# Performance work log

Measured on AMD Instinct MI355X. Metric: run time of the kernel, lower is better.

The kernel has to match this reference:

```python
import jax, jax.numpy as jnp
import numpy as np

B, NUM_USERS, NUM_ITEMS = 128, 10000, 8192
HID, LAT, NEMB, NQ, NRES = 256, 64, 512, 4, 2
CC = 0.25


def conv1d(x, w, b, stride, pad):
    # x: [N, C_in, L], w: [C_out, C_in, K] (torch Conv1d layout)
    out = jax.lax.conv_general_dilated(
        x, w, window_strides=(stride,), padding=[(pad, pad)],
        dimension_numbers=('NCH', 'OIH', 'NCH'))
    return out + b[None, :, None]


def convT1d(x, w, b, stride, pad):
    # w: [C_in, C_out, K] (torch ConvTranspose1d layout); equivalent conv with
    # flipped kernel, lhs dilation = stride, padding = K-1-pad.
    k = w.shape[-1]
    w_conv = jnp.flip(w, -1).transpose(1, 0, 2)  # [C_out, C_in, K]
    p = k - 1 - pad
    out = jax.lax.conv_general_dilated(
        x, w_conv, window_strides=(1,), padding=[(p, p)],
        lhs_dilation=(stride,), dimension_numbers=('NCH', 'OIH', 'NCH'))
    return out + b[None, :, None]


def res_block(x, w1, b1, w2, b2):
    out = jax.nn.relu(conv1d(x, w1, b1, 1, 1))
    out = conv1d(out, w2, b2, 1, 0)
    return jax.nn.relu(out + x)


def vq_step(inputs, codebook):
    # inputs: [B, LAT, L]; faithful to torch: view(-1, embedding_dim) row-major
    flat = inputs.reshape(-1, codebook.shape[1])  # [M, 64]
    dist = (jnp.sum(flat ** 2, axis=1, keepdims=True)
            + jnp.sum(codebook ** 2, axis=1)
            - 2.0 * flat @ codebook.T)  # [M, NEMB]
    idx = jnp.argmin(dist, axis=1)  # [M]
    quant = codebook[idx].reshape(inputs.shape)  # gather == onehot @ codebook
    e_loss = jnp.mean((jax.lax.stop_gradient(quant) - inputs) ** 2)
    q_loss = jnp.mean((quant - jax.lax.stop_gradient(inputs)) ** 2)
    loss = q_loss + CC * e_loss
    quant_st = inputs + jax.lax.stop_gradient(quant - inputs)  # straight-through
    counts = jnp.zeros((codebook.shape[0],), jnp.float32).at[idx].add(1.0)
    avg = counts / flat.shape[0]
    perp = jnp.exp(-jnp.sum(avg * jnp.log(avg + 1e-10)))
    return quant_st, loss, perp


def setup_inputs() -> dict:
    key = jax.random.key(0)
    ks = iter(jax.random.split(key, 32))
    nk = lambda: next(ks)
    w = lambda shape: (jax.random.normal(nk(), shape, jnp.float32) * 0.05)
    inp = {
        'user_ids': jax.random.randint(nk(), (B,), 0, NUM_USERS),
        'interaction_matrix': jax.random.uniform(nk(), (NUM_USERS, NUM_ITEMS), jnp.float32),
        'enc_conv_w': w((HID, 1, 4)), 'enc_conv_b': jnp.zeros((HID,), jnp.float32),
        'enc_res_w1': w((NRES, HID, HID, 3)), 'enc_res_b1': jnp.zeros((NRES, HID), jnp.float32),
        'enc_res_w2': w((NRES, HID, HID, 1)), 'enc_res_b2': jnp.zeros((NRES, HID), jnp.float32),
        'enc_final_w': w((LAT, HID, 3)), 'enc_final_b': jnp.zeros((LAT,), jnp.float32),
        'codebooks': jax.random.uniform(nk(), (NQ, NEMB, LAT), jnp.float32,
                                        minval=-1.0 / NEMB, maxval=1.0 / NEMB),
        'dec_convT_w': w((LAT, HID, 4)), 'dec_convT_b': jnp.zeros((HID,), jnp.float32),
        'dec_res_w1': w((NRES, HID, HID, 3)), 'dec_res_b1': jnp.zeros((NRES, HID), jnp.float32),
        'dec_res_w2': w((NRES, HID, HID, 1)), 'dec_res_b2': jnp.zeros((NRES, HID), jnp.float32),
        'dec_finalT_w': w((HID, 1, 3)), 'dec_finalT_b': jnp.zeros((1,), jnp.float32),
        'out_proj_w': (jax.random.normal(nk(), (NUM_ITEMS, NUM_ITEMS), jnp.float32)
                       * (1.0 / np.sqrt(NUM_ITEMS))),
        'out_proj_b': jnp.zeros((NUM_ITEMS,), jnp.float32),
    }
    return inp


def reference(user_ids, interaction_matrix, enc_conv_w, enc_conv_b,
              enc_res_w1, enc_res_b1, enc_res_w2, enc_res_b2,
              enc_final_w, enc_final_b, codebooks,
              dec_convT_w, dec_convT_b, dec_res_w1, dec_res_b1,
              dec_res_w2, dec_res_b2, dec_finalT_w, dec_finalT_b,
              out_proj_w, out_proj_b):
    x = interaction_matrix[user_ids][:, None, :]  # [B, 1, NUM_ITEMS]; dropout in eval mode = identity
    h = jax.nn.relu(conv1d(x, enc_conv_w, enc_conv_b, 2, 1))  # [B, HID, L]
    for i in range(NRES):
        h = res_block(h, enc_res_w1[i], enc_res_b1[i], enc_res_w2[i], enc_res_b2[i])
    z_e = conv1d(h, enc_final_w, enc_final_b, 1, 1)  # [B, LAT, L]

    residual = z_e
    z_q = jnp.zeros_like(z_e)
    vq_loss = jnp.float32(0.0)
    perps = []
    for q in range(NQ):
        quant, loss, perp = vq_step(residual, codebooks[q])
        residual = residual - quant
        z_q = z_q + quant
        vq_loss = vq_loss + loss
        perps.append(perp)
    perplexity = jnp.mean(jnp.stack(perps))

    d = jax.nn.relu(convT1d(z_q, dec_convT_w, dec_convT_b, 2, 1))  # [B, HID, NUM_ITEMS]
    for i in range(NRES):
        d = res_block(d, dec_res_w1[i], dec_res_b1[i], dec_res_w2[i], dec_res_b2[i])
    d = convT1d(d, dec_finalT_w, dec_finalT_b, 1, 1)[:, 0, :]  # [B, NUM_ITEMS]
    recon = d @ out_proj_w.T + out_proj_b
    return recon, vq_loss, perplexity
```

## Files before the change

kernel.cpp:

```cpp
#include <hip/hip_runtime.h>
#include <math.h>

#define NB 128
#define NITEMS 8192
#define NHID 256
#define NLAT 64
#define NEMB_ 512
#define NQ_ 4
#define LENC 4096
#define LDEC 8192
#define NROWS 524288
#define VQ_NELEM 33554432.0f
#define KC_ 4

typedef unsigned short u16;
typedef __attribute__((ext_vector_type(8))) short bf16x8;
typedef __attribute__((ext_vector_type(4))) float f32x4;

__device__ __forceinline__ u16 f2b(float f){
  unsigned u = __float_as_uint(f);
  unsigned r = (u + 0x7FFFu + ((u>>16)&1u)) >> 16;
  return (u16)r;
}
__device__ __forceinline__ float b2f(u16 h){
  return __uint_as_float(((unsigned)h)<<16);
}

__global__ void k_zero(float* __restrict__ p, int n){
  int i = blockIdx.x*256 + threadIdx.x;
  if(i < n) p[i] = 0.f;
}

__global__ void k_gather(const int* __restrict__ uid, const float* __restrict__ mat,
                         float* __restrict__ x){
  int b = blockIdx.y;
  int i = blockIdx.x*256 + threadIdx.x;
  x[(size_t)b*NITEMS + i] = mat[(size_t)uid[b]*NITEMS + i];
}

__global__ void k_packw(const float* __restrict__ w, u16* __restrict__ wb,
                        int CO, int CI, int K){
  int idx = blockIdx.x*256 + threadIdx.x;
  int n = CO*CI*K;
  if(idx >= n) return;
  int k  = idx % K;
  int ci = (idx / K) % CI;
  int co = idx / (K*CI);
  wb[((size_t)k*CO + co)*CI + ci] = f2b(w[idx]);
}

__global__ void k_packwT(const float* __restrict__ w, u16* __restrict__ wb){
  int idx = blockIdx.x*256 + threadIdx.x;
  if(idx >= 64*256*4) return;
  int k  = idx % 4;
  int co = (idx / 4) % 256;
  int ci = idx / (4*256);
  wb[((size_t)k*256 + co)*64 + ci] = f2b(w[idx]);
}

__global__ void k_cbsplit(const float* __restrict__ cb, u16* __restrict__ h,
                          u16* __restrict__ l){
  int idx = blockIdx.x*256 + threadIdx.x;
  float v = -2.0f*cb[idx];
  u16 hh = f2b(v);
  h[idx] = hh;
  l[idx] = f2b(v - b2f(hh));
}

__global__ void k_cbnorm(const float* __restrict__ cb, float* __restrict__ cb2){
  int idx = blockIdx.x*256 + threadIdx.x;
  if(idx >= NQ_*NEMB_) return;
  const float* p = cb + (size_t)idx*64;
  float s = 0.f;
  #pragma unroll
  for(int d=0; d<64; d++) s = fmaf(p[d], p[d], s);
  cb2[idx] = s;
}

__global__ void k_packdv(const float* __restrict__ d, u16* __restrict__ h,
                         u16* __restrict__ l){
  int i = blockIdx.x*256 + threadIdx.x;
  float v = d[i];
  u16 hh = f2b(v);
  h[i] = hh;
  l[i] = f2b(v - b2f(hh));
}

__global__ __launch_bounds__(256) void k_enc0(
    const float* __restrict__ x, const float* __restrict__ w,
    const float* __restrict__ bias, u16* __restrict__ out){
  const int co = threadIdx.x;
  const int b  = blockIdx.y;
  const int l0 = blockIdx.x*16;
  const float* xr = x + (size_t)b*NITEMS;
  float4 wv = *(const float4*)&w[co*4];
  float bv = bias[co];
  for(int dl=0; dl<16; dl++){
    int l = l0 + dl;
    int i0 = 2*l - 1;
    float x0 = (i0 >= 0) ? xr[i0] : 0.f;
    float x1 = xr[i0+1];
    float x2 = xr[i0+2];
    float x3 = (i0+3 < NITEMS) ? xr[i0+3] : 0.f;
    float acc = bv;
    acc = fmaf(wv.x, x0, acc); acc = fmaf(wv.y, x1, acc);
    acc = fmaf(wv.z, x2, acc); acc = fmaf(wv.w, x3, acc);
    out[((size_t)(b*LENC + l))*NHID + co] = f2b(fmaxf(acc, 0.f));
  }
}

#define LP 40
template<int CIN, int COUT, int KK, int WM, int WN, int RELU, int RES, int CHF>
__global__ __launch_bounds__(256) void k_cgemm(
    const u16* __restrict__ in, const u16* __restrict__ wb,
    const float* __restrict__ bias, const u16* __restrict__ res,
    void* __restrict__ outv, int L){
  constexpr int CO_T = WM*64;
  constexpr int LT   = WN*64;
  constexpr int PAD  = (KK-1)/2;
  constexpr int RXS  = LT + KK - 1;
  __shared__ __align__(16) u16 sx[RXS][LP];
  __shared__ __align__(16) u16 sw[KK][CO_T][LP];

  const int tid = threadIdx.x;
  const int bb  = blockIdx.z;
  const int co0 = blockIdx.y*CO_T;
  const int l0  = blockIdx.x*LT;
  const int wave = tid>>6, lane = tid&63;
  const int wm = wave % WM, wn = wave / WM;
  const int quad = lane>>4, l16 = lane&15;

  f32x4 acc[4][4];
  #pragma unroll
  for(int m=0;m<4;m++)
    #pragma unroll
    for(int n=0;n<4;n++) acc[m][n] = (f32x4){0.f,0.f,0.f,0.f};

  for(int cib=0; cib<CIN; cib+=32){
    for(int s=tid; s<RXS*4; s+=256){
      int row = s>>2, ch = s&3;
      int l = l0 - PAD + row;
      int4 v;
      if(l >= 0 && l < L)
        v = *(const int4*)(in + ((size_t)(bb*L + l))*CIN + cib + ch*8);
      else
        v = make_int4(0,0,0,0);
      *(int4*)&sx[row][ch*8] = v;
    }
    for(int s=tid; s<KK*CO_T*4; s+=256){
      int row = s>>2, ch = s&3;
      int kk = row / CO_T, cr = row % CO_T;
      int4 v = *(const int4*)(wb + ((size_t)(kk*COUT + co0 + cr))*CIN + cib + ch*8);
      *(int4*)&sw[kk][cr][ch*8] = v;
    }
    __syncthreads();
    #pragma unroll
    for(int kk=0; kk<KK; kk++){
      bf16x8 af[4];
      #pragma unroll
      for(int m=0;m<4;m++)
        af[m] = *(const bf16x8*)&sw[kk][wm*64 + m*16 + l16][quad*8];
      #pragma unroll
      for(int n=0;n<4;n++){
        bf16x8 bf = *(const bf16x8*)&sx[wn*64 + n*16 + l16 + kk][quad*8];
        #pragma unroll
        for(int m=0;m<4;m++)
          acc[m][n] = __builtin_amdgcn_mfma_f32_16x16x32_bf16(af[m], bf, acc[m][n], 0,0,0);
      }
    }
    __syncthreads();
  }

  #pragma unroll
  for(int m=0;m<4;m++){
    int co4 = co0 + wm*64 + m*16 + quad*4;
    float4 bv = *(const float4*)&bias[co4];
    #pragma unroll
    for(int n=0;n<4;n++){
      int l = l0 + wn*64 + n*16 + l16;
      float v0 = acc[m][n][0] + bv.x;
      float v1 = acc[m][n][1] + bv.y;
      float v2 = acc[m][n][2] + bv.z;
      float v3 = acc[m][n][3] + bv.w;
      if(RES){
        ushort4 rv = *(const ushort4*)(res + ((size_t)(bb*L + l))*COUT + co4);
        v0 += b2f(rv.x); v1 += b2f(rv.y); v2 += b2f(rv.z); v3 += b2f(rv.w);
      }
      if(RELU){
        v0 = fmaxf(v0,0.f); v1 = fmaxf(v1,0.f); v2 = fmaxf(v2,0.f); v3 = fmaxf(v3,0.f);
      }
      if(CHF){
        float* of = (float*)outv;
        of[((size_t)(bb*COUT + co4+0))*L + l] = v0;
        of[((size_t)(bb*COUT + co4+1))*L + l] = v1;
        of[((size_t)(bb*COUT + co4+2))*L + l] = v2;
        of[((size_t)(bb*COUT + co4+3))*L + l] = v3;
      }else{
        u16* ob = (u16*)outv;
        ushort4 o;
        o.x = f2b(v0); o.y = f2b(v1); o.z = f2b(v2); o.w = f2b(v3);
        *(ushort4*)(ob + ((size_t)(bb*L + l))*COUT + co4) = o;
      }
    }
  }
}

__global__ __launch_bounds__(256) void k_vq(
    const float* __restrict__ z_e, const float* __restrict__ cb,
    const u16* __restrict__ cbh, const u16* __restrict__ cbl,
    const float* __restrict__ cb2,
    float* __restrict__ z_q, float* __restrict__ loss, int* __restrict__ counts){
  __shared__ int hist[NQ_][NEMB_];
  __shared__ float sloss[NQ_];
  const int tid = threadIdx.x;
  for(int i=tid;i<NQ_*NEMB_;i+=256) (&hist[0][0])[i]=0;
  if(tid < NQ_) sloss[tid] = 0.f;
  __syncthreads();

  const int lane = tid & 63, wave = tid >> 6;
  const int quad = lane >> 4, l16 = lane & 15;
  const size_t row0 = (size_t)blockIdx.x*128 + (size_t)wave*32;

  bf16x8 vbh[2][2], vbl[2][2];
  float qa[2][2][8];
  #pragma unroll
  for(int bt=0;bt<2;bt++){
    #pragma unroll
    for(int ks=0;ks<2;ks++){
      const float* zp = z_e + (row0 + bt*16 + l16)*64 + ks*32 + quad*8;
      float4 v0 = *(const float4*)zp;
      float4 v1 = *(const float4*)(zp+4);
      float f[8] = {v0.x,v0.y,v0.z,v0.w,v1.x,v1.y,v1.z,v1.w};
      #pragma unroll
      for(int j=0;j<8;j++){
        u16 h = f2b(f[j]);
        vbh[bt][ks][j] = (short)h;
        vbl[bt][ks][j] = (short)f2b(f[j] - b2f(h));
        qa[bt][ks][j] = 0.f;
      }
    }
  }

  #pragma unroll 1
  for(int q=0;q<NQ_;q++){
    const u16* Ah = cbh + (size_t)q*NEMB_*64 + (size_t)l16*64 + quad*8;
    const u16* Al = cbl + (size_t)q*NEMB_*64 + (size_t)l16*64 + quad*8;
    const float* c2q = cb2 + q*NEMB_;

    float rq0 = 0.f, rq1 = 0.f;
    #pragma unroll
    for(int ks=0;ks<2;ks++)
      #pragma unroll
      for(int j=0;j<8;j++){
        float r0 = b2f((u16)vbh[0][ks][j]) + b2f((u16)vbl[0][ks][j]);
        float r1 = b2f((u16)vbh[1][ks][j]) + b2f((u16)vbl[1][ks][j]);
        rq0 = fmaf(r0,r0,rq0); rq1 = fmaf(r1,r1,rq1);
      }

    float best0 = 3.0e38f, best1 = 3.0e38f;
    int bi0 = 0, bi1 = 0;

    bf16x8 cah0 = *(const bf16x8*)(Ah);
    bf16x8 cah1 = *(const bf16x8*)(Ah + 32);
    bf16x8 cal0 = *(const bf16x8*)(Al);
    bf16x8 cal1 = *(const bf16x8*)(Al + 32);
    #pragma unroll 1
    for(int t=0;t<32;t++){
      int tn = (t < 31) ? (t+1) : 31;
      const u16* nh = Ah + (size_t)tn*1024;
      const u16* nl = Al + (size_t)tn*1024;
      bf16x8 nah0 = *(const bf16x8*)(nh);
      bf16x8 nah1 = *(const bf16x8*)(nh + 32);
      bf16x8 nal0 = *(const bf16x8*)(nl);
      bf16x8 nal1 = *(const bf16x8*)(nl + 32);

      f32x4 acc0 = (f32x4){0.f,0.f,0.f,0.f};
      f32x4 acc1 = (f32x4){0.f,0.f,0.f,0.f};
      acc0 = __builtin_amdgcn_mfma_f32_16x16x32_bf16(cah0, vbh[0][0], acc0, 0,0,0);
      acc1 = __builtin_amdgcn_mfma_f32_16x16x32_bf16(cah0, vbh[1][0], acc1, 0,0,0);
      acc0 = __builtin_amdgcn_mfma_f32_16x16x32_bf16(cah0, vbl[0][0], acc0, 0,0,0);
      acc1 = __builtin_amdgcn_mfma_f32_16x16x32_bf16(cah0, vbl[1][0], acc1, 0,0,0);
      acc0 = __builtin_amdgcn_mfma_f32_16x16x32_bf16(cal0, vbh[0][0], acc0, 0,0,0);
      acc1 = __builtin_amdgcn_mfma_f32_16x16x32_bf16(cal0, vbh[1][0], acc1, 0,0,0);
      acc0 = __builtin_amdgcn_mfma_f32_16x16x32_bf16(cah1, vbh[0][1], acc0, 0,0,0);
      acc1 = __builtin_amdgcn_mfma_f32_16x16x32_bf16(cah1, vbh[1][1], acc1, 0,0,0);
      acc0 = __builtin_amdgcn_mfma_f32_16x16x32_bf16(cah1, vbl[0][1], acc0, 0,0,0);
      acc1 = __builtin_amdgcn_mfma_f32_16x16x32_bf16(cah1, vbl[1][1], acc1, 0,0,0);
      acc0 = __builtin_amdgcn_mfma_f32_16x16x32_bf16(cal1, vbh[0][1], acc0, 0,0,0);
      acc1 = __builtin_amdgcn_mfma_f32_16x16x32_bf16(cal1, vbh[1][1], acc1, 0,0,0);

      float4 c2v = *(const float4*)(c2q + t*16 + quad*4);
      float c2a[4] = {c2v.x, c2v.y, c2v.z, c2v.w};
      #pragma unroll
      for(int i=0;i<4;i++){
        int code = t*16 + quad*4 + i;
        float d0 = acc0[i] + c2a[i];
        float d1 = acc1[i] + c2a[i];
        if(d0 < best0){ best0 = d0; bi0 = code; }
        if(d1 < best1){ best1 = d1; bi1 = code; }
      }
      cah0 = nah0; cah1 = nah1; cal0 = nal0; cal1 = nal1;
    }

    #pragma unroll
    for(int off=16; off<=32; off<<=1){
      float ob0 = __shfl_xor(best0, off); int oi0 = __shfl_xor(bi0, off);
      float ob1 = __shfl_xor(best1, off); int oi1 = __shfl_xor(bi1, off);
      if(ob0 < best0 || (ob0 == best0 && oi0 < bi0)){ best0 = ob0; bi0 = oi0; }
      if(ob1 < best1 || (ob1 == best1 && oi1 < bi1)){ best1 = ob1; bi1 = oi1; }
      rq0 += __shfl_xor(rq0, off);
      rq1 += __shfl_xor(rq1, off);
    }

    float v = (rq0 + best0) + (rq1 + best1);
    #pragma unroll
    for(int off=1; off<=8; off<<=1) v += __shfl_xor(v, off);
    if(lane == 0) atomicAdd(&sloss[q], v);
    if(quad == 0){
      atomicAdd(&hist[q][bi0], 1);
      atomicAdd(&hist[q][bi1], 1);
    }

    #pragma unroll
    for(int bt=0;bt<2;bt++){
      int bi = bt ? bi1 : bi0;
      const float* cp = cb + ((size_t)q*NEMB_ + bi)*64 + quad*8;
      #pragma unroll
      for(int ks=0;ks<2;ks++){
        float4 c0 = *(const float4*)(cp + ks*32);
        float4 c1 = *(const float4*)(cp + ks*32 + 4);
        float cf[8] = {c0.x,c0.y,c0.z,c0.w,c1.x,c1.y,c1.z,c1.w};
        #pragma unroll
        for(int j=0;j<8;j++){
          float r = b2f((u16)vbh[bt][ks][j]) + b2f((u16)vbl[bt][ks][j]) - cf[j];
          u16 h = f2b(r);
          vbh[bt][ks][j] = (short)h;
          vbl[bt][ks][j] = (short)f2b(r - b2f(h));
          qa[bt][ks][j] += cf[j];
        }
      }
    }
  }

  #pragma unroll
  for(int bt=0;bt<2;bt++)
    #pragma unroll
    for(int ks=0;ks<2;ks++){
      float* zp = z_q + (row0 + bt*16 + l16)*64 + ks*32 + quad*8;
      float4 w0 = {qa[bt][ks][0], qa[bt][ks][1], qa[bt][ks][2], qa[bt][ks][3]};
      float4 w1 = {qa[bt][ks][4], qa[bt][ks][5], qa[bt][ks][6], qa[bt][ks][7]};
      *(float4*)zp = w0;
      *(float4*)(zp+4) = w1;
    }

  __syncthreads();
  if(tid < NQ_) atomicAdd(&loss[tid], sloss[tid]);
  for(int i=tid;i<NQ_*NEMB_;i+=256){
    int v = (&hist[0][0])[i];
    if(v) atomicAdd(&counts[i], v);
  }
}

__global__ __launch_bounds__(256) void k_convT(
    const float* __restrict__ zq, const u16* __restrict__ wb4,
    const float* __restrict__ bias, u16* __restrict__ out){
  __shared__ __align__(16) u16 sxT[66][LP];
  __shared__ __align__(16) u16 sw4[4][128][LP];
  const int tid = threadIdx.x;
  const int bb  = blockIdx.z;
  const int co0 = blockIdx.y*128;
  const int t0  = blockIdx.x*64;
  const int wave = tid>>6, lane = tid&63;
  const int wm = wave & 1, wn = wave >> 1;
  const int quad = lane>>4, l16 = lane&15;

  f32x4 ae[4][2], ao[4][2];
  #pragma unroll
  for(int m=0;m<4;m++)
    #pragma unroll
    for(int n=0;n<2;n++){ ae[m][n]=(f32x4){0,0,0,0}; ao[m][n]=(f32x4){0,0,0,0}; }

  for(int cib=0; cib<NLAT; cib+=32){
    for(int s=tid; s<66*32; s+=256){
      int ci = s/66, tt = s%66;
      int t = t0 - 1 + tt;
      float v = 0.f;
      if(t >= 0 && t < LENC) v = zq[((size_t)(bb*NLAT + cib + ci))*LENC + t];
      sxT[tt][ci] = f2b(v);
    }
    for(int s=tid; s<4*128*4; s+=256){
      int row = s>>2, ch = s&3;
      int tap = row>>7, cr = row&127;
      int4 v = *(const int4*)(wb4 + ((size_t)(tap*NHID + co0 + cr))*NLAT + cib + ch*8);
      *(int4*)&sw4[tap][cr][ch*8] = v;
    }
    __syncthreads();
    #pragma unroll
    for(int m=0;m<4;m++){
      int crow = wm*64 + m*16 + l16;
      bf16x8 a0 = *(const bf16x8*)&sw4[0][crow][quad*8];
      bf16x8 a1 = *(const bf16x8*)&sw4[1][crow][quad*8];
      bf16x8 a2 = *(const bf16x8*)&sw4[2][crow][quad*8];
      bf16x8 a3 = *(const bf16x8*)&sw4[3][crow][quad*8];
      #pragma unroll
      for(int n=0;n<2;n++){
        int off = wn*32 + n*16 + l16;
        bf16x8 bm = *(const bf16x8*)&sxT[off  ][quad*8];
        bf16x8 b0 = *(const bf16x8*)&sxT[off+1][quad*8];
        bf16x8 bp = *(const bf16x8*)&sxT[off+2][quad*8];
        ae[m][n] = __builtin_amdgcn_mfma_f32_16x16x32_bf16(a1, b0, ae[m][n], 0,0,0);
        ae[m][n] = __builtin_amdgcn_mfma_f32_16x16x32_bf16(a3, bm, ae[m][n], 0,0,0);
        ao[m][n] = __builtin_amdgcn_mfma_f32_16x16x32_bf16(a2, b0, ao[m][n], 0,0,0);
        ao[m][n] = __builtin_amdgcn_mfma_f32_16x16x32_bf16(a0, bp, ao[m][n], 0,0,0);
      }
    }
    __syncthreads();
  }

  #pragma unroll
  for(int m=0;m<4;m++){
    int co4 = co0 + wm*64 + m*16 + quad*4;
    float4 bv = *(const float4*)&bias[co4];
    #pragma unroll
    for(int n=0;n<2;n++){
      int t = t0 + wn*32 + n*16 + l16;
      int je = 2*t, jo = 2*t+1;
      ushort4 oe, oo;
      oe.x = f2b(fmaxf(ae[m][n][0]+bv.x, 0.f));
      oe.y = f2b(fmaxf(ae[m][n][1]+bv.y, 0.f));
      oe.z = f2b(fmaxf(ae[m][n][2]+bv.z, 0.f));
      oe.w = f2b(fmaxf(ae[m][n][3]+bv.w, 0.f));
      oo.x = f2b(fmaxf(ao[m][n][0]+bv.x, 0.f));
      oo.y = f2b(fmaxf(ao[m][n][1]+bv.y, 0.f));
      oo.z = f2b(fmaxf(ao[m][n][2]+bv.z, 0.f));
      oo.w = f2b(fmaxf(ao[m][n][3]+bv.w, 0.f));
      *(ushort4*)(out + ((size_t)(bb*LDEC + je))*NHID + co4) = oe;
      *(ushort4*)(out + ((size_t)(bb*LDEC + jo))*NHID + co4) = oo;
    }
  }
}

__global__ __launch_bounds__(256) void k_finalT(
    const u16* __restrict__ in, const float* __restrict__ w,
    const float* __restrict__ bias, float* __restrict__ out){
  __shared__ u16 sd[66][258];
  __shared__ float red[4][64];
  const int tid = threadIdx.x;
  const int j0 = blockIdx.x*64;
  const int bb = blockIdx.y;
  for(int s=tid; s<66*32; s+=256){
    int row = s>>5, ch = s&31;
    int l = j0 - 1 + row;
    int4 v = make_int4(0,0,0,0);
    if(l >= 0 && l < LDEC)
      v = *(const int4*)(in + ((size_t)(bb*LDEC + l))*NHID + ch*8);
    int* dst = (int*)&sd[row][ch*8];
    dst[0]=v.x; dst[1]=v.y; dst[2]=v.z; dst[3]=v.w;
  }
  __syncthreads();
  const int jl = tid & 63;
  const int part = tid >> 6;
  float acc = 0.f;
  for(int ci=0; ci<64; ci++){
    int cg = part*64 + ci;
    float w0 = w[cg*3+2], w1 = w[cg*3+1], w2 = w[cg*3+0];
    acc = fmaf(w0, b2f(sd[jl  ][cg]), acc);
    acc = fmaf(w1, b2f(sd[jl+1][cg]), acc);
    acc = fmaf(w2, b2f(sd[jl+2][cg]), acc);
  }
  red[part][jl] = acc;
  __syncthreads();
  if(tid < 64)
    out[(size_t)bb*NITEMS + j0 + tid] =
      bias[0] + red[0][tid] + red[1][tid] + red[2][tid] + red[3][tid];
}

__global__ __launch_bounds__(256) void k_opmm(
    const u16* __restrict__ dvh, const u16* __restrict__ dvl,
    const float* __restrict__ Wm, float* __restrict__ part){
  const int tid = threadIdx.x;
  const int wave = tid>>6, lane = tid&63;
  const int quad = lane>>4, l16 = lane&15;
  const int wb_ = wave & 1;
  const int wn_ = wave >> 1;
  const int n0 = blockIdx.x*64;
  const int kz = blockIdx.y;
  const int n_wave = n0 + wn_*32;

  f32x4 acc[4][2];
  #pragma unroll
  for(int bt=0;bt<4;bt++)
    #pragma unroll
    for(int nt=0;nt<2;nt++) acc[bt][nt] = (f32x4){0.f,0.f,0.f,0.f};

  const size_t abase = (size_t)(wb_*64 + l16)*NITEMS + quad*8;
  const size_t wrow  = (size_t)(n_wave + l16)*NITEMS + quad*8;
  const int kbase = kz*(NITEMS/KC_);

  #pragma unroll 2
  for(int t=0; t<(NITEMS/KC_)/32; t++){
    const int k = kbase + t*32;
    bf16x8 ah[4], al[4];
    #pragma unroll
    for(int bt=0;bt<4;bt++){
      ah[bt] = *(const bf16x8*)(dvh + abase + (size_t)bt*16*NITEMS + k);
      al[bt] = *(const bf16x8*)(dvl + abase + (size_t)bt*16*NITEMS + k);
    }
    #pragma unroll
    for(int nt=0;nt<2;nt++){
      const float* wp = Wm + wrow + (size_t)nt*16*NITEMS + k;
      float4 wa = *(const float4*)wp;
      float4 wc = *(const float4*)(wp+4);
      float f[8] = {wa.x,wa.y,wa.z,wa.w,wc.x,wc.y,wc.z,wc.w};
      bf16x8 wh, wl;
      #pragma unroll
      for(int j=0;j<8;j++){
        u16 h = f2b(f[j]);
        wh[j] = (short)h;
        wl[j] = (short)f2b(f[j] - b2f(h));
      }
      #pragma unroll
      for(int bt=0;bt<4;bt++){
        acc[bt][nt] = __builtin_amdgcn_mfma_f32_16x16x32_bf16(ah[bt], wh, acc[bt][nt], 0,0,0);
        acc[bt][nt] = __builtin_amdgcn_mfma_f32_16x16x32_bf16(al[bt], wh, acc[bt][nt], 0,0,0);
        acc[bt][nt] = __builtin_amdgcn_mfma_f32_16x16x32_bf16(ah[bt], wl, acc[bt][nt], 0,0,0);
        acc[bt][nt] = __builtin_amdgcn_mfma_f32_16x16x32_bf16(al[bt], wl, acc[bt][nt], 0,0,0);
      }
    }
  }

  float* pp = part + (size_t)kz*NB*NITEMS;
  #pragma unroll
  for(int bt=0;bt<4;bt++){
    const int brow = wb_*64 + bt*16 + quad*4;
    #pragma unroll
    for(int nt=0;nt<2;nt++){
      const int n = n_wave + nt*16 + l16;
      #pragma unroll
      for(int i=0;i<4;i++)
        pp[(size_t)(brow+i)*NITEMS + n] = acc[bt][nt][i];
    }
  }
}

__global__ __launch_bounds__(256) void k_opred(
    const float* __restrict__ part, const float* __restrict__ bias,
    float* __restrict__ out){
  const size_t i = ((size_t)blockIdx.x*256 + threadIdx.x)*4;
  float4 s = *(const float4*)&bias[(int)(i & (NITEMS-1))];
  #pragma unroll
  for(int kz=0;kz<KC_;kz++){
    float4 p = *(const float4*)&part[(size_t)kz*NB*NITEMS + i];
    s.x+=p.x; s.y+=p.y; s.z+=p.z; s.w+=p.w;
  }
  *(float4*)&out[i] = s;
}

__global__ void k_finalize(const float* __restrict__ loss, const int* __restrict__ counts,
                           float* __restrict__ out){
  __shared__ float sh[512];
  const int tid = threadIdx.x;
  float perp_sum = 0.f;
  for(int q=0;q<NQ_;q++){
    float avg = (float)counts[q*NEMB_+tid] / (float)NROWS;
    sh[tid] = avg*logf(avg + 1e-10f);
    __syncthreads();
    for(int s=256;s>0;s>>=1){ if(tid<s) sh[tid]+=sh[tid+s]; __syncthreads(); }
    if(tid==0) perp_sum += expf(-sh[0]);
    __syncthreads();
  }
  if(tid==0){
    float vl = 0.f;
    for(int q=0;q<NQ_;q++) vl += 1.25f*loss[q]/VQ_NELEM;
    out[0] = vl;
    out[1] = perp_sum/(float)NQ_;
  }
}

extern "C" void kernel_launch(void* const* d_in, const int* in_sizes, int n_in,
                              void* d_out, int out_size, void* d_ws, size_t ws_size,
                              hipStream_t stream){
  (void)in_sizes; (void)n_in; (void)out_size;
  const int*   uid   = (const int*)d_in[0];
  const float* mat   = (const float*)d_in[1];
  const float* ec_w  = (const float*)d_in[2];
  const float* ec_b  = (const float*)d_in[3];
  const float* er_w1 = (const float*)d_in[4];
  const float* er_b1 = (const float*)d_in[5];
  const float* er_w2 = (const float*)d_in[6];
  const float* er_b2 = (const float*)d_in[7];
  const float* ef_w  = (const float*)d_in[8];
  const float* ef_b  = (const float*)d_in[9];
  const float* cb    = (const float*)d_in[10];
  const float* dt_w  = (const float*)d_in[11];
  const float* dt_b  = (const float*)d_in[12];
  const float* dr_w1 = (const float*)d_in[13];
  const float* dr_b1 = (const float*)d_in[14];
  const float* dr_w2 = (const float*)d_in[15];
  const float* dr_b2 = (const float*)d_in[16];
  const float* df_w  = (const float*)d_in[17];
  const float* df_b  = (const float*)d_in[18];
  const float* op_w  = (const float*)d_in[19];
  const float* op_b  = (const float*)d_in[20];
  float* outp = (float*)d_out;

  float* W = (float*)d_ws;
  size_t o = 0;
  float* xg    = W + o; o += (size_t)NB*NITEMS;
  float* dvec  = W + o; o += (size_t)NB*NITEMS;
  u16* wb3e0 = (u16*)(W + o); o += 3*NHID*NHID/2;
  u16* wb3e1 = (u16*)(W + o); o += 3*NHID*NHID/2;
  u16* wb3d0 = (u16*)(W + o); o += 3*NHID*NHID/2;
  u16* wb3d1 = (u16*)(W + o); o += 3*NHID*NHID/2;
  u16* wbF   = (u16*)(W + o); o += 3*NLAT*NHID/2;
  u16* wb1e0 = (u16*)(W + o); o += NHID*NHID/2;
  u16* wb1e1 = (u16*)(W + o); o += NHID*NHID/2;
  u16* wb1d0 = (u16*)(W + o); o += NHID*NHID/2;
  u16* wb1d1 = (u16*)(W + o); o += NHID*NHID/2;
  u16* wbT   = (u16*)(W + o); o += 4*NLAT*NHID/2;
  u16* cbh   = (u16*)(W + o); o += (size_t)NQ_*NEMB_*64/2;
  u16* cbl   = (u16*)(W + o); o += (size_t)NQ_*NEMB_*64/2;
  float* cb2   = W + o; o += NQ_*NEMB_;
  float* lossb = W + o; o += 4;
  int*   counts= (int*)(W + o); o += NQ_*NEMB_;
  u16* dvh   = (u16*)(W + o); o += (size_t)NB*NITEMS/2;
  u16* dvl   = (u16*)(W + o); o += (size_t)NB*NITEMS/2;
  float* partb = W + o; o += (size_t)KC_*NB*NITEMS;
  const size_t fixedF = o;

  const size_t perBF = (size_t)LDEC*NHID/2;
  size_t availF = ws_size/sizeof(float) > fixedF ? ws_size/sizeof(float) - fixedF : 0;
  int CB = 128;
  while(CB > 1 && (size_t)CB*2*perBF > availF) CB >>= 1;

  k_zero<<<(4 + NQ_*NEMB_ + 255)/256,256,0,stream>>>(lossb, 4 + NQ_*NEMB_);

  k_packw<<<(3*NHID*NHID+255)/256,256,0,stream>>>(er_w1,             wb3e0, NHID, NHID, 3);
  k_packw<<<(3*NHID*NHID+255)/256,256,0,stream>>>(er_w1+3*NHID*NHID, wb3e1, NHID, NHID, 3);
  k_packw<<<(3*NHID*NHID+255)/256,256,0,stream>>>(dr_w1,             wb3d0, NHID, NHID, 3);
  k_packw<<<(3*NHID*NHID+255)/256,256,0,stream>>>(dr_w1+3*NHID*NHID, wb3d1, NHID, NHID, 3);
  k_packw<<<(3*NLAT*NHID+255)/256,256,0,stream>>>(ef_w,              wbF,   NLAT, NHID, 3);
  k_packw<<<(NHID*NHID+255)/256,256,0,stream>>>(er_w2,               wb1e0, NHID, NHID, 1);
  k_packw<<<(NHID*NHID+255)/256,256,0,stream>>>(er_w2+NHID*NHID,     wb1e1, NHID, NHID, 1);
  k_packw<<<(NHID*NHID+255)/256,256,0,stream>>>(dr_w2,               wb1d0, NHID, NHID, 1);
  k_packw<<<(NHID*NHID+255)/256,256,0,stream>>>(dr_w2+NHID*NHID,     wb1d1, NHID, NHID, 1);
  k_packwT<<<(4*NLAT*NHID+255)/256,256,0,stream>>>(dt_w, wbT);
  k_cbsplit<<<(NQ_*NEMB_*64)/256,256,0,stream>>>(cb, cbh, cbl);
  k_cbnorm<<<(NQ_*NEMB_+255)/256,256,0,stream>>>(cb, cb2);

  k_gather<<<dim3(NITEMS/256, NB),256,0,stream>>>(uid, mat, xg);

  u16* D0b = (u16*)(W + fixedF);
  u16* D1b = D0b + (size_t)CB*LDEC*NHID;

  for(int c0 = 0; c0 < NB; c0 += CB){
    u16* E0 = D0b;
    u16* E1 = D0b + (size_t)CB*LENC*NHID;
    float* z_e = (float*)D1b;
    float* z_q = z_e + (size_t)CB*NLAT*LENC;
    const float* xgc = xg + (size_t)c0*NITEMS;
    float* dvc = dvec + (size_t)c0*NITEMS;

    k_enc0<<<dim3(LENC/16, CB),256,0,stream>>>(xgc, ec_w, ec_b, E0);
    k_cgemm<256,256,3,2,2,1,0,0><<<dim3(LENC/128, 2, CB),256,0,stream>>>(E0, wb3e0, er_b1,      nullptr, E1, LENC);
    k_cgemm<256,256,1,2,2,1,1,0><<<dim3(LENC/128, 2, CB),256,0,stream>>>(E1, wb1e0, er_b2,      E0,      E0, LENC);
    k_cgemm<256,256,3,2,2,1,0,0><<<dim3(LENC/128, 2, CB),256,0,stream>>>(E0, wb3e1, er_b1+NHID, nullptr, E1, LENC);
    k_cgemm<256,256,1,2,2,1,1,0><<<dim3(LENC/128, 2, CB),256,0,stream>>>(E1, wb1e1, er_b2+NHID, E0,      E0, LENC);
    k_cgemm<256, 64,3,1,4,0,0,1><<<dim3(LENC/256, 1, CB),256,0,stream>>>(E0, wbF,   ef_b,       nullptr, z_e, LENC);

    k_vq<<<CB*32,256,0,stream>>>(z_e, cb, cbh, cbl, cb2, z_q, lossb, counts);

    k_convT<<<dim3(LENC/64, 2, CB),256,0,stream>>>(z_q, wbT, dt_b, D0b);
    k_cgemm<256,256,3,2,2,1,0,0><<<dim3(LDEC/128, 2, CB),256,0,stream>>>(D0b, wb3d0, dr_b1,      nullptr, D1b, LDEC);
    k_cgemm<256,256,1,2,2,1,1,0><<<dim3(LDEC/128, 2, CB),256,0,stream>>>(D1b, wb1d0, dr_b2,      D0b,     D0b, LDEC);
    k_cgemm<256,256,3,2,2,1,0,0><<<dim3(LDEC/128, 2, CB),256,0,stream>>>(D0b, wb3d1, dr_b1+NHID, nullptr, D1b, LDEC);
    k_cgemm<256,256,1,2,2,1,1,0><<<dim3(LDEC/128, 2, CB),256,0,stream>>>(D1b, wb1d1, dr_b2+NHID, D0b,     D0b, LDEC);
    k_finalT<<<dim3(LDEC/64, CB),256,0,stream>>>(D0b, df_w, df_b, dvc);
  }

  k_packdv<<<NB*NITEMS/256,256,0,stream>>>(dvec, dvh, dvl);
  k_opmm<<<dim3(NITEMS/64, KC_),256,0,stream>>>(dvh, dvl, op_w, partb);
  k_opred<<<NB*NITEMS/1024,256,0,stream>>>(partb, op_b, outp);
  k_finalize<<<1,512,0,stream>>>(lossb, counts, outp + (size_t)NB*NITEMS);
}
```

Baseline: 6.859 ms.

## Process 64 rows per wave in VQ with triple-buffered codebook loads

The VQ kernel now handles four 16-row tiles per wave instead of two, so each codebook fragment load feeds twice as many MFMAs, and the grid is halved to match. Codebook tiles are prefetched through a three-stage rotating register buffer instead of single-step double buffering. The per-row quantized accumulator is dropped; z_q is rebuilt at the end as z_e minus the final residual, which trades registers for an extra reload of z_e. Register pressure rises and occupancy may fall, and the reconstructed z_q may differ slightly in rounding from the old running sum.

New measurement: 6.477 ms. 1.06x faster.

```diff
diff --git a/kernel.cpp b/kernel.cpp
--- a/kernel.cpp
+++ b/kernel.cpp
@@ -205,6 +205,57 @@
   }
 }
 
+#define VQ_LOADT(S, T) { \
+  const u16* nh_ = Ah + (size_t)(T)*1024; \
+  const u16* nl_ = Al + (size_t)(T)*1024; \
+  s_h0[S] = *(const bf16x8*)(nh_); \
+  s_h1[S] = *(const bf16x8*)(nh_ + 32); \
+  s_l0[S] = *(const bf16x8*)(nl_); \
+  s_l1[S] = *(const bf16x8*)(nl_ + 32); \
+}
+
+#define VQ_DOT(S, T) { \
+  f32x4 ac0=(f32x4){0.f,0.f,0.f,0.f}, ac1=ac0, ac2=ac0, ac3=ac0; \
+  ac0 = __builtin_amdgcn_mfma_f32_16x16x32_bf16(s_h0[S], vbh[0][0], ac0,0,0,0); \
+  ac1 = __builtin_amdgcn_mfma_f32_16x16x32_bf16(s_h0[S], vbh[1][0], ac1,0,0,0); \
+  ac2 = __builtin_amdgcn_mfma_f32_16x16x32_bf16(s_h0[S], vbh[2][0], ac2,0,0,0); \
+  ac3 = __builtin_amdgcn_mfma_f32_16x16x32_bf16(s_h0[S], vbh[3][0], ac3,0,0,0); \
+  ac0 = __builtin_amdgcn_mfma_f32_16x16x32_bf16(s_h0[S], vbl[0][0], ac0,0,0,0); \
+  ac1 = __builtin_amdgcn_mfma_f32_16x16x32_bf16(s_h0[S], vbl[1][0], ac1,0,0,0); \
+  ac2 = __builtin_amdgcn_mfma_f32_16x16x32_bf16(s_h0[S], vbl[2][0], ac2,0,0,0); \
+  ac3 = __builtin_amdgcn_mfma_f32_16x16x32_bf16(s_h0[S], vbl[3][0], ac3,0,0,0); \
+  ac0 = __builtin_amdgcn_mfma_f32_16x16x32_bf16(s_l0[S], vbh[0][0], ac0,0,0,0); \
+  ac1 = __builtin_amdgcn_mfma_f32_16x16x32_bf16(s_l0[S], vbh[1][0], ac1,0,0,0); \
+  ac2 = __builtin_amdgcn_mfma_f32_16x16x32_bf16(s_l0[S], vbh[2][0], ac2,0,0,0); \
+  ac3 = __builtin_amdgcn_mfma_f32_16x16x32_bf16(s_l0[S], vbh[3][0], ac3,0,0,0); \
+  ac0 = __builtin_amdgcn_mfma_f32_16x16x32_bf16(s_h1[S], vbh[0][1], ac0,0,0,0); \
+  ac1 = __builtin_amdgcn_mfma_f32_16x16x32_bf16(s_h1[S], vbh[1][1], ac1,0,0,0); \
+  ac2 = __builtin_amdgcn_mfma_f32_16x16x32_bf16(s_h1[S], vbh[2][1], ac2,0,0,0); \
+  ac3 = __builtin_amdgcn_mfma_f32_16x16x32_bf16(s_h1[S], vbh[3][1], ac3,0,0,0); \
+  ac0 = __builtin_amdgcn_mfma_f32_16x16x32_bf16(s_h1[S], vbl[0][1], ac0,0,0,0); \
+  ac1 = __builtin_amdgcn_mfma_f32_16x16x32_bf16(s_h1[S], vbl[1][1], ac1,0,0,0); \
+  ac2 = __builtin_amdgcn_mfma_f32_16x16x32_bf16(s_h1[S], vbl[2][1], ac2,0,0,0); \
+  ac3 = __builtin_amdgcn_mfma_f32_16x16x32_bf16(s_h1[S], vbl[3][1], ac3,0,0,0); \
+  ac0 = __builtin_amdgcn_mfma_f32_16x16x32_bf16(s_l1[S], vbh[0][1], ac0,0,0,0); \
+  ac1 = __builtin_amdgcn_mfma_f32_16x16x32_bf16(s_l1[S], vbh[1][1], ac1,0,0,0); \
+  ac2 = __builtin_amdgcn_mfma_f32_16x16x32_bf16(s_l1[S], vbh[2][1], ac2,0,0,0); \
+  ac3 = __builtin_amdgcn_mfma_f32_16x16x32_bf16(s_l1[S], vbh[3][1], ac3,0,0,0); \
+  float4 c2v = *(const float4*)(c2q + (T)*16 + quad*4); \
+  const float* c2a = (const float*)&c2v; \
+  _Pragma("unroll") \
+  for(int i_=0;i_<4;i_++){ \
+    int code = (T)*16 + quad*4 + i_; \
+    float d0 = ac0[i_] + c2a[i_]; \
+    float d1 = ac1[i_] + c2a[i_]; \
+    float d2 = ac2[i_] + c2a[i_]; \
+    float d3 = ac3[i_] + c2a[i_]; \
+    if(d0 < best[0]){ best[0]=d0; bi[0]=code; } \
+    if(d1 < best[1]){ best[1]=d1; bi[1]=code; } \
+    if(d2 < best[2]){ best[2]=d2; bi[2]=code; } \
+    if(d3 < best[3]){ best[3]=d3; bi[3]=code; } \
+  } \
+}
+
 __global__ __launch_bounds__(256) void k_vq(
     const float* __restrict__ z_e, const float* __restrict__ cb,
     const u16* __restrict__ cbh, const u16* __restrict__ cbl,
@@ -219,12 +270,11 @@
 
   const int lane = tid & 63, wave = tid >> 6;
   const int quad = lane >> 4, l16 = lane & 15;
-  const size_t row0 = (size_t)blockIdx.x*128 + (size_t)wave*32;
-
-  bf16x8 vbh[2][2], vbl[2][2];
-  float qa[2][2][8];
-  #pragma unroll
-  for(int bt=0;bt<2;bt++){
+  const size_t row0 = (size_t)blockIdx.x*256 + (size_t)wave*64;
+
+  bf16x8 vbh[4][2], vbl[4][2];
+  #pragma unroll
+  for(int bt=0;bt<4;bt++){
     #pragma unroll
     for(int ks=0;ks<2;ks++){
       const float* zp = z_e + (row0 + bt*16 + l16)*64 + ks*32 + quad*8;
@@ -236,7 +286,6 @@
         u16 h = f2b(f[j]);
         vbh[bt][ks][j] = (short)h;
         vbl[bt][ks][j] = (short)f2b(f[j] - b2f(h));
-        qa[bt][ks][j] = 0.f;
       }
     }
   }
@@ -247,84 +296,59 @@
     const u16* Al = cbl + (size_t)q*NEMB_*64 + (size_t)l16*64 + quad*8;
     const float* c2q = cb2 + q*NEMB_;
 
-    float rq0 = 0.f, rq1 = 0.f;
-    #pragma unroll
-    for(int ks=0;ks<2;ks++)
-      #pragma unroll
-      for(int j=0;j<8;j++){
-        float r0 = b2f((u16)vbh[0][ks][j]) + b2f((u16)vbl[0][ks][j]);
-        float r1 = b2f((u16)vbh[1][ks][j]) + b2f((u16)vbl[1][ks][j]);
-        rq0 = fmaf(r0,r0,rq0); rq1 = fmaf(r1,r1,rq1);
-      }
-
-    float best0 = 3.0e38f, best1 = 3.0e38f;
-    int bi0 = 0, bi1 = 0;
-
-    bf16x8 cah0 = *(const bf16x8*)(Ah);
-    bf16x8 cah1 = *(const bf16x8*)(Ah + 32);
-    bf16x8 cal0 = *(const bf16x8*)(Al);
-    bf16x8 cal1 = *(const bf16x8*)(Al + 32);
+    float rq[4];
+    #pragma unroll
+    for(int bt=0;bt<4;bt++){
+      float s = 0.f;
+      #pragma unroll
+      for(int ks=0;ks<2;ks++)
+        #pragma unroll
+        for(int j=0;j<8;j++){
+          float r = b2f((u16)vbh[bt][ks][j]) + b2f((u16)vbl[bt][ks][j]);
+          s = fmaf(r,r,s);
+        }
+      rq[bt] = s;
+    }
+
+    float best[4] = {3.0e38f,3.0e38f,3.0e38f,3.0e38f};
+    int   bi[4]   = {0,0,0,0};
+
+    bf16x8 s_h0[3], s_h1[3], s_l0[3], s_l1[3];
+    VQ_LOADT(0, 0);
+    VQ_LOADT(1, 1);
     #pragma unroll 1
-    for(int t=0;t<32;t++){
-      int tn = (t < 31) ? (t+1) : 31;
-      const u16* nh = Ah + (size_t)tn*1024;
-      const u16* nl = Al + (size_t)tn*1024;
-      bf16x8 nah0 = *(const bf16x8*)(nh);
-      bf16x8 nah1 = *(const bf16x8*)(nh + 32);
-      bf16x8 nal0 = *(const bf16x8*)(nl);
-      bf16x8 nal1 = *(const bf16x8*)(nl + 32);
-
-      f32x4 acc0 = (f32x4){0.f,0.f,0.f,0.f};
-      f32x4 acc1 = (f32x4){0.f,0.f,0.f,0.f};
-      acc0 = __builtin_amdgcn_mfma_f32_16x16x32_bf16(cah0, vbh[0][0], acc0, 0,0,0);
-      acc1 = __builtin_amdgcn_mfma_f32_16x16x32_bf16(cah0, vbh[1][0], acc1, 0,0,0);
-      acc0 = __builtin_amdgcn_mfma_f32_16x16x32_bf16(cah0, vbl[0][0], acc0, 0,0,0);
-      acc1 = __builtin_amdgcn_mfma_f32_16x16x32_bf16(cah0, vbl[1][0], acc1, 0,0,0);
-      acc0 = __builtin_amdgcn_mfma_f32_16x16x32_bf16(cal0, vbh[0][0], acc0, 0,0,0);
-      acc1 = __builtin_amdgcn_mfma_f32_16x16x32_bf16(cal0, vbh[1][0], acc1, 0,0,0);
-      acc0 = __builtin_amdgcn_mfma_f32_16x16x32_bf16(cah1, vbh[0][1], acc0, 0,0,0);
-      acc1 = __builtin_amdgcn_mfma_f32_16x16x32_bf16(cah1, vbh[1][1], acc1, 0,0,0);
-      acc0 = __builtin_amdgcn_mfma_f32_16x16x32_bf16(cah1, vbl[0][1], acc0, 0,0,0);
-      acc1 = __builtin_amdgcn_mfma_f32_16x16x32_bf16(cah1, vbl[1][1], acc1, 0,0,0);
-      acc0 = __builtin_amdgcn_mfma_f32_16x16x32_bf16(cal1, vbh[0][1], acc0, 0,0,0);
-      acc1 = __builtin_amdgcn_mfma_f32_16x16x32_bf16(cal1, vbh[1][1], acc1, 0,0,0);
-
-      float4 c2v = *(const float4*)(c2q + t*16 + quad*4);
-      float c2a[4] = {c2v.x, c2v.y, c2v.z, c2v.w};
-      #pragma unroll
-      for(int i=0;i<4;i++){
-        int code = t*16 + quad*4 + i;
-        float d0 = acc0[i] + c2a[i];
-        float d1 = acc1[i] + c2a[i];
-        if(d0 < best0){ best0 = d0; bi0 = code; }
-        if(d1 < best1){ best1 = d1; bi1 = code; }
-      }
-      cah0 = nah0; cah1 = nah1; cal0 = nal0; cal1 = nal1;
-    }
-
-    #pragma unroll
-    for(int off=16; off<=32; off<<=1){
-      float ob0 = __shfl_xor(best0, off); int oi0 = __shfl_xor(bi0, off);
-      float ob1 = __shfl_xor(best1, off); int oi1 = __shfl_xor(bi1, off);
-      if(ob0 < best0 || (ob0 == best0 && oi0 < bi0)){ best0 = ob0; bi0 = oi0; }
-      if(ob1 < best1 || (ob1 == best1 && oi1 < bi1)){ best1 = ob1; bi1 = oi1; }
-      rq0 += __shfl_xor(rq0, off);
-      rq1 += __shfl_xor(rq1, off);
-    }
-
-    float v = (rq0 + best0) + (rq1 + best1);
+    for(int t=0; t<30; t+=3){
+      VQ_LOADT(2, t+2);  VQ_DOT(0, t);
+      VQ_LOADT(0, t+3);  VQ_DOT(1, t+1);
+      VQ_LOADT(1, t+4);  VQ_DOT(2, t+2);
+    }
+    VQ_DOT(0, 30);
+    VQ_DOT(1, 31);
+
+    #pragma unroll
+    for(int bt=0;bt<4;bt++){
+      #pragma unroll
+      for(int off=16; off<=32; off<<=1){
+        float ob = __shfl_xor(best[bt], off); int oi = __shfl_xor(bi[bt], off);
+        if(ob < best[bt] || (ob == best[bt] && oi < bi[bt])){ best[bt]=ob; bi[bt]=oi; }
+        rq[bt] += __shfl_xor(rq[bt], off);
+      }
+    }
+
+    float v = (rq[0]+best[0]) + (rq[1]+best[1]) + (rq[2]+best[2]) + (rq[3]+best[3]);
     #pragma unroll
     for(int off=1; off<=8; off<<=1) v += __shfl_xor(v, off);
     if(lane == 0) atomicAdd(&sloss[q], v);
     if(quad == 0){
-      atomicAdd(&hist[q][bi0], 1);
-      atomicAdd(&hist[q][bi1], 1);
-    }
-
-    #pragma unroll
-    for(int bt=0;bt<2;bt++){
-      int bi = bt ? bi1 : bi0;
-      const float* cp = cb + ((size_t)q*NEMB_ + bi)*64 + quad*8;
+      atomicAdd(&hist[q][bi[0]], 1);
+      atomicAdd(&hist[q][bi[1]], 1);
+      atomicAdd(&hist[q][bi[2]], 1);
+      atomicAdd(&hist[q][bi[3]], 1);
+    }
+
+    #pragma unroll
+    for(int bt=0;bt<4;bt++){
+      const float* cp = cb + ((size_t)q*NEMB_ + bi[bt])*64 + quad*8;
       #pragma unroll
       for(int ks=0;ks<2;ks++){
         float4 c0 = *(const float4*)(cp + ks*32);
@@ -336,22 +360,30 @@
           u16 h = f2b(r);
           vbh[bt][ks][j] = (short)h;
           vbl[bt][ks][j] = (short)f2b(r - b2f(h));
-          qa[bt][ks][j] += cf[j];
         }
       }
     }
   }
 
   #pragma unroll
-  for(int bt=0;bt<2;bt++)
+  for(int bt=0;bt<4;bt++){
     #pragma unroll
     for(int ks=0;ks<2;ks++){
-      float* zp = z_q + (row0 + bt*16 + l16)*64 + ks*32 + quad*8;
-      float4 w0 = {qa[bt][ks][0], qa[bt][ks][1], qa[bt][ks][2], qa[bt][ks][3]};
-      float4 w1 = {qa[bt][ks][4], qa[bt][ks][5], qa[bt][ks][6], qa[bt][ks][7]};
-      *(float4*)zp = w0;
-      *(float4*)(zp+4) = w1;
-    }
+      const float* zp = z_e + (row0 + bt*16 + l16)*64 + ks*32 + quad*8;
+      float*       qp = z_q + (row0 + bt*16 + l16)*64 + ks*32 + quad*8;
+      float4 z0 = *(const float4*)zp;
+      float4 z1 = *(const float4*)(zp+4);
+      float zf[8] = {z0.x,z0.y,z0.z,z0.w,z1.x,z1.y,z1.z,z1.w};
+      float o[8];
+      #pragma unroll
+      for(int j=0;j<8;j++)
+        o[j] = zf[j] - (b2f((u16)vbh[bt][ks][j]) + b2f((u16)vbl[bt][ks][j]));
+      float4 w0 = {o[0],o[1],o[2],o[3]};
+      float4 w1 = {o[4],o[5],o[6],o[7]};
+      *(float4*)qp = w0;
+      *(float4*)(qp+4) = w1;
+    }
+  }
 
   __syncthreads();
   if(tid < NQ_) atomicAdd(&loss[tid], sloss[tid]);
@@ -668,7 +700,7 @@
     k_cgemm<256,256,1,2,2,1,1,0><<<dim3(LENC/128, 2, CB),256,0,stream>>>(E1, wb1e1, er_b2+NHID, E0,      E0, LENC);
     k_cgemm<256, 64,3,1,4,0,0,1><<<dim3(LENC/256, 1, CB),256,0,stream>>>(E0, wbF,   ef_b,       nullptr, z_e, LENC);
 
-    k_vq<<<CB*32,256,0,stream>>>(z_e, cb, cbh, cbl, cb2, z_q, lossb, counts);
+    k_vq<<<CB*16,256,0,stream>>>(z_e, cb, cbh, cbl, cb2, z_q, lossb, counts);
 
     k_convT<<<dim3(LENC/64, 2, CB),256,0,stream>>>(z_q, wbT, dt_b, D0b);
     k_cgemm<256,256,3,2,2,1,0,0><<<dim3(LDEC/128, 2, CB),256,0,stream>>>(D0b, wb3d0, dr_b1,      nullptr, D1b, LDEC);
```
